# Kernel tuning notes

Hardware: AMD Instinct MI355X
Metric: run time of the kernel (lower is better)

The kernel has to match this reference:

```python
import jax, jax.numpy as jnp
import numpy as np

FEAT_DIM = 2048
HIDDEN = 1024
ATTN_DIM = 512
BATCH = 128
NPOS = 196


def setup_inputs() -> dict:
    key = jax.random.key(0)
    ks = jax.random.split(key, 8)
    # Linear layers use kaiming-uniform-ish init; plain scaled normal is fine for a numeric baseline.
    def lin(k, fan_in, fan_out):
        k1, k2 = jax.random.split(k)
        bound = 1.0 / np.sqrt(fan_in)
        W = jax.random.uniform(k1, (fan_out, fan_in), jnp.float32, -bound, bound)
        b = jax.random.uniform(k2, (fan_out,), jnp.float32, -bound, bound)
        return W, b
    We, be = lin(ks[0], FEAT_DIM, ATTN_DIM)
    Wd, bd = lin(ks[1], HIDDEN, ATTN_DIM)
    Wf, bf = lin(ks[2], ATTN_DIM, 1)
    encoder_out = jax.random.normal(ks[3], (BATCH, NPOS, FEAT_DIM), jnp.float32)
    hidden = jax.random.normal(ks[4], (BATCH, HIDDEN), jnp.float32)
    return {
        "encoder_out": encoder_out,
        "hidden": hidden,
        "We": We, "be": be,
        "Wd": Wd, "bd": bd,
        "Wf": Wf, "bf": bf,
    }


def reference(encoder_out, hidden, We, be, Wd, bd, Wf, bf):
    # enc: [B, P, A]; dec: [B, 1, A]
    enc = jnp.einsum('bpf,af->bpa', encoder_out, We) + be
    dec = (jnp.einsum('bh,ah->ba', hidden, Wd) + bd)[:, None, :]
    scores = jnp.tanh(enc + dec)
    # full_attn: [A] -> scalar per position; Wf has shape [1, A]
    scores = jnp.einsum('bpa,a->bp', scores, Wf[0]) + bf[0]
    alpha = jax.nn.softmax(scores, axis=1)  # [B, P]
    context = jnp.einsum('bpf,bp->bf', encoder_out, alpha)  # [B, F]
    return context, alpha
```

## Files before the change

### kernel.cpp

```cpp
#include <hip/hip_runtime.h>
#include <hip/hip_bf16.h>

typedef __bf16 bf16x8 __attribute__((ext_vector_type(8)));
typedef float f32x4 __attribute__((ext_vector_type(4)));

#define FEAT 2048
#define HID  1024
#define AD   512
#define NB   128
#define NP   196
#define MROWS (NB * NP)
#define BM 128
#define BK 64
#define NSTEP (FEAT / BK)

__global__ __launch_bounds__(256) void pack_we_k(const float* __restrict__ We,
                                                 __bf16* __restrict__ Bp) {
    int t = blockIdx.x * 256 + threadIdx.x;
    int a  = t >> 8;
    int f0 = (t & 255) << 3;
    const float4* src = reinterpret_cast<const float4*>(We + ((size_t)a << 11) + f0);
    float4 x0 = src[0], x1 = src[1];
    int nt = a >> 4, r = a & 15;
    int kt = f0 >> 5, g = (f0 >> 3) & 3;
    size_t off = (((size_t)(kt * 32 + nt) * 64) + (r + (g << 4))) << 3;
    union { __bf16 h[8]; bf16x8 v; } u;
    u.h[0] = (__bf16)x0.x; u.h[1] = (__bf16)x0.y; u.h[2] = (__bf16)x0.z; u.h[3] = (__bf16)x0.w;
    u.h[4] = (__bf16)x1.x; u.h[5] = (__bf16)x1.y; u.h[6] = (__bf16)x1.z; u.h[7] = (__bf16)x1.w;
    *reinterpret_cast<bf16x8*>(Bp + off) = u.v;
}

__global__ __launch_bounds__(256) void dec_k(const float* __restrict__ hidden,
                                             const float* __restrict__ Wd,
                                             const float* __restrict__ bd,
                                             const float* __restrict__ be,
                                             float* __restrict__ decb) {
    __shared__ float w[8][1028];
    const int tid = threadIdx.x;
    const int n0 = blockIdx.x << 3;
    const float4* wsrc = reinterpret_cast<const float4*>(Wd + ((size_t)n0 << 10));
    #pragma unroll
    for (int i = 0; i < 8; ++i)
        *reinterpret_cast<float4*>(&w[i][tid << 2]) = wsrc[(i << 8) + tid];
    __syncthreads();
    const int nl = tid & 7, b0 = tid >> 3;
    float acc[4] = {0.f, 0.f, 0.f, 0.f};
    const float4* wp = reinterpret_cast<const float4*>(&w[nl][0]);
    #pragma unroll 2
    for (int k4 = 0; k4 < 256; ++k4) {
        float4 wv = wp[k4];
        #pragma unroll
        for (int i = 0; i < 4; ++i) {
            const float4 h = reinterpret_cast<const float4*>(
                hidden + ((size_t)(b0 + (i << 5)) << 10))[k4];
            acc[i] = fmaf(wv.x, h.x, acc[i]);
            acc[i] = fmaf(wv.y, h.y, acc[i]);
            acc[i] = fmaf(wv.z, h.z, acc[i]);
            acc[i] = fmaf(wv.w, h.w, acc[i]);
        }
    }
    const float bias = bd[n0 + nl] + be[n0 + nl];
    #pragma unroll
    for (int i = 0; i < 4; ++i)
        decb[(size_t)(b0 + (i << 5)) * AD + n0 + nl] = acc[i] + bias;
}

__device__ __forceinline__ void store16(char* d0, char* d1,
                                        float4 a, float4 b, float4 c, float4 d) {
    union { __bf16 h[8]; bf16x8 v; } u0, u1;
    u0.h[0]=(__bf16)a.x; u0.h[1]=(__bf16)a.y; u0.h[2]=(__bf16)a.z; u0.h[3]=(__bf16)a.w;
    u0.h[4]=(__bf16)b.x; u0.h[5]=(__bf16)b.y; u0.h[6]=(__bf16)b.z; u0.h[7]=(__bf16)b.w;
    u1.h[0]=(__bf16)c.x; u1.h[1]=(__bf16)c.y; u1.h[2]=(__bf16)c.z; u1.h[3]=(__bf16)c.w;
    u1.h[4]=(__bf16)d.x; u1.h[5]=(__bf16)d.y; u1.h[6]=(__bf16)d.z; u1.h[7]=(__bf16)d.w;
    *reinterpret_cast<bf16x8*>(d0) = u0.v;
    *reinterpret_cast<bf16x8*>(d1) = u1.v;
}

__device__ __forceinline__ void do_step(const char* buf, const __bf16* __restrict__ bs,
                                        int rc0, int rc1, int lr, f32x4 acc[8][4]) {
    #pragma unroll
    for (int kt2 = 0; kt2 < 2; ++kt2) {
        const __bf16* bk = bs + kt2 * 16384;
        bf16x8 b0 = *reinterpret_cast<const bf16x8*>(bk);
        bf16x8 b1 = *reinterpret_cast<const bf16x8*>(bk + 512);
        bf16x8 b2 = *reinterpret_cast<const bf16x8*>(bk + 1024);
        bf16x8 b3 = *reinterpret_cast<const bf16x8*>(bk + 1536);
        const int rc = kt2 ? rc1 : rc0;
        #pragma unroll
        for (int mt = 0; mt < 8; ++mt) {
            bf16x8 a = *reinterpret_cast<const bf16x8*>(buf + (mt * 16 + lr) * 128 + rc);
            acc[mt][0] = __builtin_amdgcn_mfma_f32_16x16x32_bf16(a, b0, acc[mt][0], 0, 0, 0);
            acc[mt][1] = __builtin_amdgcn_mfma_f32_16x16x32_bf16(a, b1, acc[mt][1], 0, 0, 0);
            acc[mt][2] = __builtin_amdgcn_mfma_f32_16x16x32_bf16(a, b2, acc[mt][2], 0, 0, 0);
            acc[mt][3] = __builtin_amdgcn_mfma_f32_16x16x32_bf16(a, b3, acc[mt][3], 0, 0, 0);
        }
    }
}

__global__ __launch_bounds__(512, 2) void enc_score_k(
        const float* __restrict__ X, const __bf16* __restrict__ Bp,
        const float* __restrict__ decb, const float* __restrict__ Wf,
        float* __restrict__ scores) {
    __shared__ char ldsA0[BM * BK * 2];
    __shared__ char ldsA1[BM * BK * 2];
    __shared__ float swave[8][BM];
    const int tid  = threadIdx.x;
    const int wave = tid >> 6, lane = tid & 63;
    const int lr = lane & 15, lg = lane >> 4;
    const int row0 = blockIdx.x * BM;

    f32x4 acc[8][4];
    #pragma unroll
    for (int mt = 0; mt < 8; ++mt) {
        #pragma unroll
        for (int j = 0; j < 4; ++j) {
            const int row = mt * 16 + lg * 4 + j;
            const int b = (unsigned)(row0 + row) / 196u;
            const float* dp = decb + (size_t)b * AD + wave * 64 + lr;
            #pragma unroll
            for (int nt = 0; nt < 4; ++nt) acc[mt][nt][j] = dp[nt * 16];
        }
    }

    const int srow = tid >> 2, sq = tid & 3;
    const float* gA = X + (size_t)(row0 + srow) * FEAT + sq * 16;
    const int swz = (srow & 7) << 4;
    char* wp0a = ldsA0 + srow * 128 + ((sq * 32) ^ swz);
    char* wp0b = ldsA0 + srow * 128 + ((sq * 32 + 16) ^ swz);
    char* wp1a = ldsA1 + srow * 128 + ((sq * 32) ^ swz);
    char* wp1b = ldsA1 + srow * 128 + ((sq * 32 + 16) ^ swz);

    const int rswz = (lr & 7) << 4;
    const int rc0 = (lg * 16) ^ rswz;
    const int rc1 = (64 + lg * 16) ^ rswz;
    const __bf16* bbase = Bp + wave * 2048 + lane * 8;

    float4 rA0, rA1, rA2, rA3, rB0, rB1, rB2, rB3;
    {   const float4* g = reinterpret_cast<const float4*>(gA);
        rA0 = g[0]; rA1 = g[1]; rA2 = g[2]; rA3 = g[3]; }
    store16(wp0a, wp0b, rA0, rA1, rA2, rA3);
    {   const float4* g = reinterpret_cast<const float4*>(gA + 64);
        rB0 = g[0]; rB1 = g[1]; rB2 = g[2]; rB3 = g[3]; }

    for (int s = 0; s < NSTEP; s += 2) {
        const bool more = (s + 2 < NSTEP);
        __syncthreads();
        if (more) {
            const float4* g = reinterpret_cast<const float4*>(gA + (size_t)(s + 2) * BK);
            rA0 = g[0]; rA1 = g[1]; rA2 = g[2]; rA3 = g[3];
        }
        do_step(ldsA0, bbase + (size_t)s * 32768, rc0, rc1, lr, acc);
        store16(wp1a, wp1b, rB0, rB1, rB2, rB3);
        __syncthreads();
        if (more) {
            const float4* g = reinterpret_cast<const float4*>(gA + (size_t)(s + 3) * BK);
            rB0 = g[0]; rB1 = g[1]; rB2 = g[2]; rB3 = g[3];
        }
        do_step(ldsA1, bbase + (size_t)(s + 1) * 32768, rc0, rc1, lr, acc);
        if (more) store16(wp0a, wp0b, rA0, rA1, rA2, rA3);
    }

    float wf[4];
    #pragma unroll
    for (int nt = 0; nt < 4; ++nt) wf[nt] = Wf[wave * 64 + nt * 16 + lr];
    #pragma unroll
    for (int mt = 0; mt < 8; ++mt) {
        #pragma unroll
        for (int j = 0; j < 4; ++j) {
            float s = 0.f;
            #pragma unroll
            for (int nt = 0; nt < 4; ++nt) {
                float x = acc[mt][nt][j];
                float e = __expf(2.0f * x);
                float t = 1.0f - 2.0f / (e + 1.0f);
                s = fmaf(t, wf[nt], s);
            }
            s += __shfl_xor(s, 1); s += __shfl_xor(s, 2);
            s += __shfl_xor(s, 4); s += __shfl_xor(s, 8);
            if (lr == 0) swave[wave][mt * 16 + lg * 4 + j] = s;
        }
    }
    __syncthreads();
    if (tid < BM) {
        float s = 0.f;
        #pragma unroll
        for (int w = 0; w < 8; ++w) s += swave[w][tid];
        scores[row0 + tid] = s;
    }
}

__global__ __launch_bounds__(64) void softmax_k(const float* __restrict__ scores,
                                                float* __restrict__ alpha) {
    const int b = blockIdx.x, lane = threadIdx.x;
    float v[4], e[4];
    float m = -3.0e38f;
    #pragma unroll
    for (int i = 0; i < 4; ++i) {
        int p = i * 64 + lane;
        v[i] = (p < NP) ? scores[b * NP + p] : -3.0e38f;
        m = fmaxf(m, v[i]);
    }
    #pragma unroll
    for (int o = 1; o < 64; o <<= 1) m = fmaxf(m, __shfl_xor(m, o));
    float s = 0.f;
    #pragma unroll
    for (int i = 0; i < 4; ++i) {
        int p = i * 64 + lane;
        e[i] = (p < NP) ? __expf(v[i] - m) : 0.f;
        s += e[i];
    }
    #pragma unroll
    for (int o = 1; o < 64; o <<= 1) s += __shfl_xor(s, o);
    const float inv = 1.0f / s;
    #pragma unroll
    for (int i = 0; i < 4; ++i) {
        int p = i * 64 + lane;
        if (p < NP) alpha[b * NP + p] = e[i] * inv;
    }
}

__global__ __launch_bounds__(128) void context_k(const float* __restrict__ X,
                                                 const float* __restrict__ alpha,
                                                 float* __restrict__ ctx) {
    __shared__ float al[NP];
    const int bid = blockIdx.x;
    const int b = 127 - (bid >> 2);
    const int chunk = bid & 3;
    const int tid = threadIdx.x;
    for (int i = tid; i < NP; i += 128) al[i] = alpha[b * NP + i];
    __syncthreads();
    const float4* Xp = reinterpret_cast<const float4*>(X + (size_t)b * NP * FEAT)
                       + chunk * 128 + tid;
    float4 a0 = {0,0,0,0}, a1 = {0,0,0,0};
    #pragma unroll 4
    for (int p = 0; p < NP; p += 2) {
        const float w0 = al[p], w1 = al[p + 1];
        const float4 x0 = Xp[(size_t)p * 512];
        const float4 x1 = Xp[(size_t)(p + 1) * 512];
        a0.x = fmaf(w0, x0.x, a0.x); a0.y = fmaf(w0, x0.y, a0.y);
        a0.z = fmaf(w0, x0.z, a0.z); a0.w = fmaf(w0, x0.w, a0.w);
        a1.x = fmaf(w1, x1.x, a1.x); a1.y = fmaf(w1, x1.y, a1.y);
        a1.z = fmaf(w1, x1.z, a1.z); a1.w = fmaf(w1, x1.w, a1.w);
    }
    float4 r; r.x = a0.x + a1.x; r.y = a0.y + a1.y; r.z = a0.z + a1.z; r.w = a0.w + a1.w;
    *reinterpret_cast<float4*>(ctx + (size_t)b * FEAT + chunk * 512 + tid * 4) = r;
}

extern "C" void kernel_launch(void* const* d_in, const int* in_sizes, int n_in,
                              void* d_out, int out_size, void* d_ws, size_t ws_size,
                              hipStream_t stream) {
    const float* enc    = (const float*)d_in[0];
    const float* hidden = (const float*)d_in[1];
    const float* We     = (const float*)d_in[2];
    const float* be     = (const float*)d_in[3];
    const float* Wd     = (const float*)d_in[4];
    const float* bd     = (const float*)d_in[5];
    const float* Wf     = (const float*)d_in[6];

    float* out   = (float*)d_out;
    float* ctx   = out;
    float* alpha = out + NB * FEAT;

    char* ws = (char*)d_ws;
    __bf16* Bp    = (__bf16*)ws;
    float*  decb  = (float*)(ws + (2u << 20));
    float*  score = (float*)(ws + (2u << 20) + (256u << 10));

    pack_we_k  <<<dim3(512), dim3(256), 0, stream>>>(We, Bp);
    dec_k      <<<dim3(64),  dim3(256), 0, stream>>>(hidden, Wd, bd, be, decb);
    enc_score_k<<<dim3(MROWS / BM), dim3(512), 0, stream>>>(enc, Bp, decb, Wf, score);
    softmax_k  <<<dim3(NB),  dim3(64),  0, stream>>>(score, alpha);
    context_k  <<<dim3(512), dim3(128), 0, stream>>>(enc, alpha, ctx);
}
```

Measured before the change: 163.4 us.

## Split encoder GEMM into half-width column tiles with smaller row tiles

Result: slower. 192.8 us (+18.0%).

```diff
diff --git a/kernel.cpp b/kernel.cpp
--- a/kernel.cpp
+++ b/kernel.cpp
@@ -10,9 +10,10 @@
 #define NB   128
 #define NP   196
 #define MROWS (NB * NP)
-#define BM 128
+#define BM 64
 #define BK 64
 #define NSTEP (FEAT / BK)
+#define NBLK (MROWS / BM * 2)
 
 __global__ __launch_bounds__(256) void pack_we_k(const float* __restrict__ We,
                                                  __bf16* __restrict__ Bp) {
@@ -77,7 +78,7 @@
 }
 
 __device__ __forceinline__ void do_step(const char* buf, const __bf16* __restrict__ bs,
-                                        int rc0, int rc1, int lr, f32x4 acc[8][4]) {
+                                        int rc0, int rc1, int lr, f32x4 acc[4][4]) {
     #pragma unroll
     for (int kt2 = 0; kt2 < 2; ++kt2) {
         const __bf16* bk = bs + kt2 * 16384;
@@ -87,7 +88,7 @@
         bf16x8 b3 = *reinterpret_cast<const bf16x8*>(bk + 1536);
         const int rc = kt2 ? rc1 : rc0;
         #pragma unroll
-        for (int mt = 0; mt < 8; ++mt) {
+        for (int mt = 0; mt < 4; ++mt) {
             bf16x8 a = *reinterpret_cast<const bf16x8*>(buf + (mt * 16 + lr) * 128 + rc);
             acc[mt][0] = __builtin_amdgcn_mfma_f32_16x16x32_bf16(a, b0, acc[mt][0], 0, 0, 0);
             acc[mt][1] = __builtin_amdgcn_mfma_f32_16x16x32_bf16(a, b1, acc[mt][1], 0, 0, 0);
@@ -97,26 +98,29 @@
     }
 }
 
-__global__ __launch_bounds__(512, 2) void enc_score_k(
+__global__ __launch_bounds__(256, 3) void enc_score_k(
         const float* __restrict__ X, const __bf16* __restrict__ Bp,
         const float* __restrict__ decb, const float* __restrict__ Wf,
-        float* __restrict__ scores) {
+        float* __restrict__ spart) {
     __shared__ char ldsA0[BM * BK * 2];
     __shared__ char ldsA1[BM * BK * 2];
-    __shared__ float swave[8][BM];
+    __shared__ float swave[4][BM];
     const int tid  = threadIdx.x;
     const int wave = tid >> 6, lane = tid & 63;
     const int lr = lane & 15, lg = lane >> 4;
-    const int row0 = blockIdx.x * BM;
-
-    f32x4 acc[8][4];
-    #pragma unroll
-    for (int mt = 0; mt < 8; ++mt) {
+    const int vbid = (blockIdx.x & 7) * (NBLK / 8) + (blockIdx.x >> 3);
+    const int rt = vbid >> 1, nh = vbid & 1;
+    const int row0 = rt * BM;
+    const int ncol0 = nh * 256 + wave * 64;
+
+    f32x4 acc[4][4];
+    #pragma unroll
+    for (int mt = 0; mt < 4; ++mt) {
         #pragma unroll
         for (int j = 0; j < 4; ++j) {
             const int row = mt * 16 + lg * 4 + j;
             const int b = (unsigned)(row0 + row) / 196u;
-            const float* dp = decb + (size_t)b * AD + wave * 64 + lr;
+            const float* dp = decb + (size_t)b * AD + ncol0 + lr;
             #pragma unroll
             for (int nt = 0; nt < 4; ++nt) acc[mt][nt][j] = dp[nt * 16];
         }
@@ -133,7 +137,7 @@
     const int rswz = (lr & 7) << 4;
     const int rc0 = (lg * 16) ^ rswz;
     const int rc1 = (64 + lg * 16) ^ rswz;
-    const __bf16* bbase = Bp + wave * 2048 + lane * 8;
+    const __bf16* bbase = Bp + (size_t)(nh * 16 + wave * 4) * 512 + lane * 8;
 
     float4 rA0, rA1, rA2, rA3, rB0, rB1, rB2, rB3;
     {   const float4* g = reinterpret_cast<const float4*>(gA);
@@ -162,9 +166,9 @@
 
     float wf[4];
     #pragma unroll
-    for (int nt = 0; nt < 4; ++nt) wf[nt] = Wf[wave * 64 + nt * 16 + lr];
-    #pragma unroll
-    for (int mt = 0; mt < 8; ++mt) {
+    for (int nt = 0; nt < 4; ++nt) wf[nt] = Wf[ncol0 + nt * 16 + lr];
+    #pragma unroll
+    for (int mt = 0; mt < 4; ++mt) {
         #pragma unroll
         for (int j = 0; j < 4; ++j) {
             float s = 0.f;
@@ -182,14 +186,12 @@
     }
     __syncthreads();
     if (tid < BM) {
-        float s = 0.f;
-        #pragma unroll
-        for (int w = 0; w < 8; ++w) s += swave[w][tid];
-        scores[row0 + tid] = s;
-    }
-}
-
-__global__ __launch_bounds__(64) void softmax_k(const float* __restrict__ scores,
+        float s = swave[0][tid] + swave[1][tid] + swave[2][tid] + swave[3][tid];
+        spart[(size_t)nh * MROWS + row0 + tid] = s;
+    }
+}
+
+__global__ __launch_bounds__(64) void softmax_k(const float* __restrict__ spart,
                                                 float* __restrict__ alpha) {
     const int b = blockIdx.x, lane = threadIdx.x;
     float v[4], e[4];
@@ -197,7 +199,7 @@
     #pragma unroll
     for (int i = 0; i < 4; ++i) {
         int p = i * 64 + lane;
-        v[i] = (p < NP) ? scores[b * NP + p] : -3.0e38f;
+        v[i] = (p < NP) ? (spart[b * NP + p] + spart[MROWS + b * NP + p]) : -3.0e38f;
         m = fmaxf(m, v[i]);
     }
     #pragma unroll
@@ -264,11 +266,11 @@
     char* ws = (char*)d_ws;
     __bf16* Bp    = (__bf16*)ws;
     float*  decb  = (float*)(ws + (2u << 20));
-    float*  score = (float*)(ws + (2u << 20) + (256u << 10));
+    float*  spart = (float*)(ws + (2u << 20) + (256u << 10));
 
     pack_we_k  <<<dim3(512), dim3(256), 0, stream>>>(We, Bp);
     dec_k      <<<dim3(64),  dim3(256), 0, stream>>>(hidden, Wd, bd, be, decb);
-    enc_score_k<<<dim3(MROWS / BM), dim3(512), 0, stream>>>(enc, Bp, decb, Wf, score);
-    softmax_k  <<<dim3(NB),  dim3(64),  0, stream>>>(score, alpha);
+    enc_score_k<<<dim3(NBLK), dim3(256), 0, stream>>>(enc, Bp, decb, Wf, spart);
+    softmax_k  <<<dim3(NB),  dim3(64),  0, stream>>>(spart, alpha);
     context_k  <<<dim3(512), dim3(128), 0, stream>>>(enc, alpha, ctx);
 }
```
